# Optimization experiments

Measured on AMD Instinct MI355X. Metric: run time of the kernel, lower is better.

## Reference

```python
import jax, jax.numpy as jnp
import numpy as np

S, B, I, H, O = 4096, 64, 14, 256, 1


def _lstm_layer(xs, W_ih, W_hh, b_ih, b_hh, h, c):
    # Precompute input contribution for all timesteps in one big GEMM.
    # xs: [S, B, D_in] -> pre: [S, B, 4H]  (PyTorch gate order: i, f, g, o)
    pre = jnp.einsum('sbd,gd->sbg', xs, W_ih) + b_ih + b_hh

    def step(carry, px):
        h, c = carry
        gates = px + h @ W_hh.T  # [B, 4H]
        i, f, g, o = jnp.split(gates, 4, axis=-1)
        i = jax.nn.sigmoid(i)
        f = jax.nn.sigmoid(f)
        g = jnp.tanh(g)
        o = jax.nn.sigmoid(o)
        c = f * c + i * g
        h = o * jnp.tanh(c)
        return (h, c), h

    (_, _), hs = jax.lax.scan(step, (h, c), pre)
    return hs  # [S, B, H]


def setup_inputs() -> dict:
    key = jax.random.key(0)
    ks = jax.random.split(key, 14)
    s = 1.0 / np.sqrt(H)  # PyTorch LSTM init scale
    u = lambda k, shape: jax.random.uniform(k, shape, jnp.float32, -s, s)
    return {
        'x': jax.random.normal(ks[0], (S, B, I), jnp.float32),
        'h0': jax.random.normal(ks[1], (2, B, H), jnp.float32),
        'c0': jax.random.normal(ks[2], (2, B, H), jnp.float32),
        'W_ih0': u(ks[3], (4 * H, I)),
        'W_hh0': u(ks[4], (4 * H, H)),
        'b_ih0': u(ks[5], (4 * H,)),
        'b_hh0': u(ks[6], (4 * H,)),
        'W_ih1': u(ks[7], (4 * H, H)),
        'W_hh1': u(ks[8], (4 * H, H)),
        'b_ih1': u(ks[9], (4 * H,)),
        'b_hh1': u(ks[10], (4 * H,)),
        'W_fc': u(ks[11], (O, H)),
        'b_fc': u(ks[12], (O,)),
    }


def reference(x, h0, c0, W_ih0, W_hh0, b_ih0, b_hh0,
              W_ih1, W_hh1, b_ih1, b_hh1, W_fc, b_fc):
    hs0 = _lstm_layer(x, W_ih0, W_hh0, b_ih0, b_hh0, h0[0], c0[0])
    # dropout=0.4 between layers applies only in train mode; eval reference -> identity
    hs1 = _lstm_layer(hs0, W_ih1, W_hh1, b_ih1, b_hh1, h0[1], c0[1])
    out = jax.nn.relu(hs1)
    return out @ W_fc.T + b_fc  # [S, B, O]
```

## Files before the change

kernel.cpp:

```cpp
#include <hip/hip_runtime.h>


#define S_LEN 4096
#define BATCH 64
#define IN_DIM 14
#define HID 256
#define GATES 1024
#define K0 288
#define LDA0 296
#define K1 512
#define LDA1 520
#define GST 260

typedef _Float16 half8 __attribute__((ext_vector_type(8)));
typedef float f32x4 __attribute__((ext_vector_type(4)));
typedef unsigned long long u64;
typedef unsigned int u32;

__device__ __forceinline__ float sigf(float z) { return 1.0f / (1.0f + __expf(-z)); }
__device__ __forceinline__ float tanhf2(float z) { return 2.0f / (1.0f + __expf(-2.0f * z)) - 1.0f; }

__device__ __forceinline__ u32 packh2(float a, float b) {
    union { _Float16 h[2]; u32 u; } q;
    q.h[0] = (_Float16)a; q.h[1] = (_Float16)b;
    return q.u;
}

__device__ __forceinline__ u64 ld64_c(const u64* p) {
    u64 r;
    asm volatile("global_load_dwordx2 %0, %1, off sc0 sc1\n\ts_waitcnt vmcnt(0)"
                 : "=&v"(r) : "v"(p) : "memory");
    return r;
}
__device__ __forceinline__ void st64_c(u64* p, u64 v) {
    asm volatile("global_store_dwordx2 %0, %1, off sc0 sc1" :: "v"(p), "v"(v) : "memory");
}
__device__ __forceinline__ u32 ld32_c(const u32* p) {
    u32 r;
    asm volatile("global_load_dword %0, %1, off sc0 sc1\n\ts_waitcnt vmcnt(0)"
                 : "=&v"(r) : "v"(p) : "memory");
    return r;
}
__device__ __forceinline__ void st32_c(u32* p, u32 v) {
    asm volatile("global_store_dword %0, %1, off sc0 sc1" :: "v"(p), "v"(v) : "memory");
}
__device__ __forceinline__ void ld64x3_c(const u64* p0, const u64* p1, const u64* p2,
                                         u64& r0, u64& r1, u64& r2) {
    asm volatile(
        "global_load_dwordx2 %0, %3, off sc0 sc1\n\t"
        "global_load_dwordx2 %1, %4, off sc0 sc1\n\t"
        "global_load_dwordx2 %2, %5, off sc0 sc1\n\t"
        "s_waitcnt vmcnt(0)"
        : "=&v"(r0), "=&v"(r1), "=&v"(r2)
        : "v"(p0), "v"(p1), "v"(p2)
        : "memory");
}
__device__ __forceinline__ void ld64x7_c(
    const u64* a0, const u64* a1, const u64* a2, const u64* a3,
    const u64* p0, const u64* p1, const u64* p2,
    u64& q0, u64& q1, u64& q2, u64& q3, u64& v0, u64& v1, u64& v2) {
    asm volatile(
        "global_load_dwordx2 %0, %7, off sc0 sc1\n\t"
        "global_load_dwordx2 %1, %8, off sc0 sc1\n\t"
        "global_load_dwordx2 %2, %9, off sc0 sc1\n\t"
        "global_load_dwordx2 %3, %10, off sc0 sc1\n\t"
        "global_load_dwordx2 %4, %11, off sc0 sc1\n\t"
        "global_load_dwordx2 %5, %12, off sc0 sc1\n\t"
        "global_load_dwordx2 %6, %13, off sc0 sc1\n\t"
        "s_waitcnt vmcnt(0)"
        : "=&v"(q0), "=&v"(q1), "=&v"(q2), "=&v"(q3), "=&v"(v0), "=&v"(v1), "=&v"(v2)
        : "v"(a0), "v"(a1), "v"(a2), "v"(a3), "v"(p0), "v"(p1), "v"(p2)
        : "memory");
}

__global__ void prep_weights(const float* __restrict__ Wih0, const float* __restrict__ Whh0,
                             const float* __restrict__ bih0, const float* __restrict__ bhh0,
                             const float* __restrict__ Wih1, const float* __restrict__ Whh1,
                             const float* __restrict__ bih1, const float* __restrict__ bhh1,
                             _Float16* __restrict__ wcat0, _Float16* __restrict__ wcat1,
                             float* __restrict__ b0, float* __restrict__ b1) {
    int idx0 = blockIdx.x * blockDim.x + threadIdx.x;
    int stride = gridDim.x * blockDim.x;
    for (int i = idx0; i < GATES * K0; i += stride) {
        int n = i / K0, k = i % K0;
        float v = 0.f;
        if (k < HID) v = Whh0[n * HID + k];
        else if (k < HID + IN_DIM) v = Wih0[n * IN_DIM + (k - HID)];
        wcat0[i] = (_Float16)v;
    }
    for (int i = idx0; i < GATES * K1; i += stride) {
        int n = i / K1, k = i % K1;
        float v = (k < HID) ? Whh1[n * HID + k] : Wih1[n * HID + (k - HID)];
        wcat1[i] = (_Float16)v;
    }
    for (int i = idx0; i < GATES; i += stride) {
        b0[i] = bih0[i] + bhh0[i];
        b1[i] = bih1[i] + bhh1[i];
    }
}

__global__ __launch_bounds__(512) void lstm_scan(
    const float* __restrict__ x, const float* __restrict__ h0g, const float* __restrict__ c0g,
    const _Float16* __restrict__ wcat0, const _Float16* __restrict__ wcat1,
    const float* __restrict__ b0, const float* __restrict__ b1,
    const float* __restrict__ wfc, const float* __restrict__ bfc,
    u64* __restrict__ h0ring, u64* __restrict__ h1ring,
    u32* __restrict__ prog, float* __restrict__ out, int R0) {
    const int bi = blockIdx.x;
    const int x7 = bi & 7;
    const int g = x7 >> 1;
    const int sub = ((x7 & 1) << 2) | (bi >> 3);
    const int L = sub >> 2;
    const int j = sub & 3;

    const int tid = threadIdx.x;
    const int w = tid >> 6;
    const int lane = tid & 63;
    const int quad = lane >> 4;
    const int col = lane & 15;
    const int c0b = g * 16;
    const int pm = tid & 15;
    const int iu = tid >> 4;
    const int pu = iu * 2;
    const int gm = tid >> 5;
    const int gu = tid & 31;

    __shared__ __align__(16) _Float16 Ash[16 * LDA1];
    __shared__ float Gsh[16 * GST];
    __shared__ float WfS[HID];
    __shared__ u32 OwnH[512];

    u64* h0w = h0ring + (size_t)g * R0 * 2048;
    u64* h1w = h1ring + (size_t)g * 4 * 2048;
    const int R0m = R0 - 1;

    int peer[3];
    { int c = 0; for (int p = 0; p < 4; ++p) if (p != j) peer[c++] = p; }

    int gbudget = 1 << 24;

    if (L == 0) {
        half8 wr[2][K0 / 32];
        float bs[2];
#pragma unroll
        for (int tt = 0; tt < 2; ++tt) {
            int t = w + 8 * tt;
            int n = (t >> 2) * 256 + j * 64 + (t & 3) * 16 + col;
            bs[tt] = b0[n];
            const _Float16* wp = wcat0 + (size_t)n * K0 + quad * 8;
#pragma unroll
            for (int kk = 0; kk < K0 / 32; ++kk) wr[tt][kk] = *(const half8*)(wp + kk * 32);
        }
        float cs0 = c0g[(size_t)(c0b + pm) * HID + j * 64 + pu];
        float cs1 = c0g[(size_t)(c0b + pm) * HID + j * 64 + pu + 1];
        {
            int m = tid >> 5, cw = tid & 31;
            const float* hp = h0g + (size_t)(c0b + m) * HID + cw * 8;
            half8 hv;
#pragma unroll
            for (int q2 = 0; q2 < 8; ++q2) hv[q2] = (_Float16)hp[q2];
            *(half8*)&Ash[m * LDA0 + cw * 8] = hv;
            if (cw >= IN_DIM) Ash[m * LDA0 + HID + cw] = (_Float16)0.f;
        }
        const int xm = tid / IN_DIM, xd = tid - xm * IN_DIM;
        if (tid < 16 * IN_DIM)
            Ash[xm * LDA0 + HID + xd] = (_Float16)x[(size_t)(c0b + xm) * IN_DIM + xd];
        __syncthreads();

        for (int s = 0; s < S_LEN; ++s) {
            float xpre = 0.f;
            if (tid < 16 * IN_DIM && s + 1 < S_LEN)
                xpre = x[((size_t)(s + 1) * BATCH + c0b + xm) * IN_DIM + xd];
            if (w == 0 && lane < 4 && (s & 7) == 0 && s + 10 > R0) {
                const u32* np = prog + g * 4 + lane;
                int tgt = s + 10 - R0;
                while ((int)ld32_c(np) < tgt && --gbudget > 0) __builtin_amdgcn_s_sleep(4);
            }
            if (s > 0) {
                const u64* base = h0w + (size_t)((s - 1) & R0m) * 2048;
                const u64* p0 = base + peer[0] * 512 + tid;
                const u64* p1 = base + peer[1] * 512 + tid;
                const u64* p2 = base + peer[2] * 512 + tid;
                u64 v0, v1, v2;
                ld64x3_c(p0, p1, p2, v0, v1, v2);
                const u32 tg = (u32)s;
                while ((u32)(v0 >> 32) != tg && --gbudget > 0) v0 = ld64_c(p0);
                while ((u32)(v1 >> 32) != tg && --gbudget > 0) v1 = ld64_c(p1);
                while ((u32)(v2 >> 32) != tg && --gbudget > 0) v2 = ld64_c(p2);
                *(u32*)&Ash[gm * LDA0 + peer[0] * 64 + 2 * gu] = (u32)v0;
                *(u32*)&Ash[gm * LDA0 + peer[1] * 64 + 2 * gu] = (u32)v1;
                *(u32*)&Ash[gm * LDA0 + peer[2] * 64 + 2 * gu] = (u32)v2;
            }
            __syncthreads();
            f32x4 acc0 = {bs[0], bs[0], bs[0], bs[0]};
            f32x4 acc1 = {bs[1], bs[1], bs[1], bs[1]};
#pragma unroll
            for (int kk = 0; kk < K0 / 32; ++kk) {
                half8 av = *(const half8*)&Ash[col * LDA0 + kk * 32 + quad * 8];
                acc0 = __builtin_amdgcn_mfma_f32_16x16x32_f16(av, wr[0][kk], acc0, 0, 0, 0);
                acc1 = __builtin_amdgcn_mfma_f32_16x16x32_f16(av, wr[1][kk], acc1, 0, 0, 0);
            }
#pragma unroll
            for (int r = 0; r < 4; ++r) {
                Gsh[(quad * 4 + r) * GST + w * 16 + col] = acc0[r];
                Gsh[(quad * 4 + r) * GST + (w + 8) * 16 + col] = acc1[r];
            }
            __syncthreads();
            {
                float iv = sigf(Gsh[pm * GST + pu]);
                float fv = sigf(Gsh[pm * GST + 64 + pu]);
                float gv = tanhf2(Gsh[pm * GST + 128 + pu]);
                float ov = sigf(Gsh[pm * GST + 192 + pu]);
                cs0 = fv * cs0 + iv * gv;
                float ha = ov * tanhf2(cs0);
                iv = sigf(Gsh[pm * GST + pu + 1]);
                fv = sigf(Gsh[pm * GST + 64 + pu + 1]);
                gv = tanhf2(Gsh[pm * GST + 128 + pu + 1]);
                ov = sigf(Gsh[pm * GST + 192 + pu + 1]);
                cs1 = fv * cs1 + iv * gv;
                float hb = ov * tanhf2(cs1);
                u32 hw = packh2(ha, hb);
                *(u32*)&Ash[pm * LDA0 + j * 64 + pu] = hw;
                st64_c(h0w + (size_t)(s & R0m) * 2048 + j * 512 + (pm * 32 + iu),
                       (u64)hw | ((u64)(u32)(s + 1) << 32));
            }
            if (tid < 16 * IN_DIM && s + 1 < S_LEN)
                Ash[xm * LDA0 + HID + xd] = (_Float16)xpre;
            __syncthreads();
        }
    } else {
        half8 wr[2][K1 / 32];
        float bs[2];
#pragma unroll
        for (int tt = 0; tt < 2; ++tt) {
            int t = w + 8 * tt;
            int n = (t >> 2) * 256 + j * 64 + (t & 3) * 16 + col;
            bs[tt] = b1[n];
            const _Float16* wp = wcat1 + (size_t)n * K1 + quad * 8;
#pragma unroll
            for (int kk = 0; kk < K1 / 32; ++kk) wr[tt][kk] = *(const half8*)(wp + kk * 32);
        }
        for (int i = tid; i < HID; i += 512) WfS[i] = wfc[i];
        const float bfcv = bfc[0];
        float cs0 = c0g[(size_t)(BATCH + c0b + pm) * HID + j * 64 + pu];
        float cs1 = c0g[(size_t)(BATCH + c0b + pm) * HID + j * 64 + pu + 1];
        {
            int m = tid >> 5, cw = tid & 31;
            const float* hp = h0g + (size_t)(BATCH + c0b + m) * HID + cw * 8;
            half8 hv;
#pragma unroll
            for (int q2 = 0; q2 < 8; ++q2) hv[q2] = (_Float16)hp[q2];
            *(half8*)&Ash[m * LDA1 + cw * 8] = hv;
        }
        u32* progself = prog + g * 4 + j;
        __syncthreads();

        for (int s = 0; s <= S_LEN; ++s) {
            if (w == 7 && s >= 2) {
                int m = 4 * j + quad;
                float fa = 0.f;
#pragma unroll
                for (int k16 = 0; k16 < 16; ++k16) {
                    float hv = (float)Ash[m * LDA1 + col + 16 * k16];
                    fa += fmaxf(hv, 0.f) * WfS[col + 16 * k16];
                }
#pragma unroll
                for (int off = 1; off < 16; off <<= 1) fa += __shfl_xor(fa, off, 16);
                if (col == 0) out[(size_t)(s - 2) * BATCH + c0b + m] = fa + bfcv;
            }
            const u64* hb = h0w + (size_t)((s < S_LEN ? s : 0) & R0m) * 2048;
            const u64* a0 = hb + tid;
            const u64* a1 = hb + 512 + tid;
            const u64* a2 = hb + 1024 + tid;
            const u64* a3 = hb + 1536 + tid;
            const u64* pb = h1w + (size_t)(((s > 0 ? s : 1) - 1) & 3) * 2048;
            const u64* p0 = pb + peer[0] * 512 + tid;
            const u64* p1 = pb + peer[1] * 512 + tid;
            const u64* p2 = pb + peer[2] * 512 + tid;
            u64 q0, q1, q2, q3, v0, v1, v2;
            ld64x7_c(a0, a1, a2, a3, p0, p1, p2, q0, q1, q2, q3, v0, v1, v2);
            if (s < S_LEN) {
                const u32 tg = (u32)(s + 1);
                while ((u32)(q0 >> 32) != tg && --gbudget > 0) q0 = ld64_c(a0);
                while ((u32)(q1 >> 32) != tg && --gbudget > 0) q1 = ld64_c(a1);
                while ((u32)(q2 >> 32) != tg && --gbudget > 0) q2 = ld64_c(a2);
                while ((u32)(q3 >> 32) != tg && --gbudget > 0) q3 = ld64_c(a3);
            }
            if (s > 0) {
                const u32 tg = (u32)s;
                while ((u32)(v0 >> 32) != tg && --gbudget > 0) v0 = ld64_c(p0);
                while ((u32)(v1 >> 32) != tg && --gbudget > 0) v1 = ld64_c(p1);
                while ((u32)(v2 >> 32) != tg && --gbudget > 0) v2 = ld64_c(p2);
            }
            __syncthreads();
            if (s > 0) {
                *(u32*)&Ash[gm * LDA1 + peer[0] * 64 + 2 * gu] = (u32)v0;
                *(u32*)&Ash[gm * LDA1 + peer[1] * 64 + 2 * gu] = (u32)v1;
                *(u32*)&Ash[gm * LDA1 + peer[2] * 64 + 2 * gu] = (u32)v2;
                *(u32*)&Ash[gm * LDA1 + j * 64 + 2 * gu] = OwnH[tid];
            }
            if (s < S_LEN) {
                *(u32*)&Ash[gm * LDA1 + HID + 0 * 64 + 2 * gu] = (u32)q0;
                *(u32*)&Ash[gm * LDA1 + HID + 1 * 64 + 2 * gu] = (u32)q1;
                *(u32*)&Ash[gm * LDA1 + HID + 2 * 64 + 2 * gu] = (u32)q2;
                *(u32*)&Ash[gm * LDA1 + HID + 3 * 64 + 2 * gu] = (u32)q3;
            }
            __syncthreads();
            if (s == S_LEN) {
                if (w == 7) {
                    int m = 4 * j + quad;
                    float fa = 0.f;
#pragma unroll
                    for (int k16 = 0; k16 < 16; ++k16) {
                        float hv = (float)Ash[m * LDA1 + col + 16 * k16];
                        fa += fmaxf(hv, 0.f) * WfS[col + 16 * k16];
                    }
#pragma unroll
                    for (int off = 1; off < 16; off <<= 1) fa += __shfl_xor(fa, off, 16);
                    if (col == 0) out[(size_t)(S_LEN - 1) * BATCH + c0b + m] = fa + bfcv;
                }
                break;
            }
            f32x4 acc0 = {bs[0], bs[0], bs[0], bs[0]};
            f32x4 acc1 = {bs[1], bs[1], bs[1], bs[1]};
#pragma unroll
            for (int kk = 0; kk < K1 / 32; ++kk) {
                half8 av = *(const half8*)&Ash[col * LDA1 + kk * 32 + quad * 8];
                acc0 = __builtin_amdgcn_mfma_f32_16x16x32_f16(av, wr[0][kk], acc0, 0, 0, 0);
                acc1 = __builtin_amdgcn_mfma_f32_16x16x32_f16(av, wr[1][kk], acc1, 0, 0, 0);
            }
#pragma unroll
            for (int r = 0; r < 4; ++r) {
                Gsh[(quad * 4 + r) * GST + w * 16 + col] = acc0[r];
                Gsh[(quad * 4 + r) * GST + (w + 8) * 16 + col] = acc1[r];
            }
            __syncthreads();
            {
                float iv = sigf(Gsh[pm * GST + pu]);
                float fv = sigf(Gsh[pm * GST + 64 + pu]);
                float gv = tanhf2(Gsh[pm * GST + 128 + pu]);
                float ov = sigf(Gsh[pm * GST + 192 + pu]);
                cs0 = fv * cs0 + iv * gv;
                float ha = ov * tanhf2(cs0);
                iv = sigf(Gsh[pm * GST + pu + 1]);
                fv = sigf(Gsh[pm * GST + 64 + pu + 1]);
                gv = tanhf2(Gsh[pm * GST + 128 + pu + 1]);
                ov = sigf(Gsh[pm * GST + 192 + pu + 1]);
                cs1 = fv * cs1 + iv * gv;
                float hb = ov * tanhf2(cs1);
                u32 hw = packh2(ha, hb);
                OwnH[pm * 32 + iu] = hw;
                st64_c(h1w + (size_t)(s & 3) * 2048 + j * 512 + (pm * 32 + iu),
                       (u64)hw | ((u64)(u32)(s + 1) << 32));
            }
            if ((s & 7) == 7 && tid == 0) st32_c(progself, (u32)(s + 1));
            __syncthreads();
        }
    }
}

extern "C" void kernel_launch(void* const* d_in, const int* in_sizes, int n_in,
                              void* d_out, int out_size, void* d_ws, size_t ws_size,
                              hipStream_t stream) {
    const float* x    = (const float*)d_in[0];
    const float* h0   = (const float*)d_in[1];
    const float* c0   = (const float*)d_in[2];
    const float* Wih0 = (const float*)d_in[3];
    const float* Whh0 = (const float*)d_in[4];
    const float* bih0 = (const float*)d_in[5];
    const float* bhh0 = (const float*)d_in[6];
    const float* Wih1 = (const float*)d_in[7];
    const float* Whh1 = (const float*)d_in[8];
    const float* bih1 = (const float*)d_in[9];
    const float* bhh1 = (const float*)d_in[10];
    const float* Wfc  = (const float*)d_in[11];
    const float* bfc  = (const float*)d_in[12];
    float* out = (float*)d_out;

    char* ws = (char*)d_ws;
    constexpr size_t OFF_WCAT0 = 0;
    constexpr size_t SZ_WCAT0 = (size_t)GATES * K0 * 2;
    constexpr size_t OFF_WCAT1 = OFF_WCAT0 + SZ_WCAT0;
    constexpr size_t SZ_WCAT1 = (size_t)GATES * K1 * 2;
    constexpr size_t OFF_B0 = OFF_WCAT1 + SZ_WCAT1;
    constexpr size_t OFF_B1 = OFF_B0 + 4096;
    constexpr size_t OFF_PROG = OFF_B1 + 4096;
    constexpr size_t OFF_H1R = OFF_PROG + 4096;
    constexpr size_t SZ_H1R = (size_t)4 * 4 * 2048 * 8;
    constexpr size_t OFF_H0R = OFF_H1R + SZ_H1R;

    _Float16* wcat0 = (_Float16*)(ws + OFF_WCAT0);
    _Float16* wcat1 = (_Float16*)(ws + OFF_WCAT1);
    float* b0 = (float*)(ws + OFF_B0);
    float* b1 = (float*)(ws + OFF_B1);
    u32* prog = (u32*)(ws + OFF_PROG);
    u64* h1ring = (u64*)(ws + OFF_H1R);

    int R0 = 128;
    while (OFF_H0R + (size_t)4 * R0 * 2048 * 8 > ws_size && R0 > 16) R0 >>= 1;
    u64* h0ring = (u64*)(ws + OFF_H0R);

    hipMemsetAsync(ws + OFF_PROG, 0,
                   (OFF_H0R - OFF_PROG) + (size_t)4 * R0 * 2048 * 8, stream);
    prep_weights<<<256, 256, 0, stream>>>(Wih0, Whh0, bih0, bhh0, Wih1, Whh1, bih1, bhh1,
                                          wcat0, wcat1, b0, b1);
    lstm_scan<<<32, 512, 0, stream>>>(x, h0, c0, wcat0, wcat1, b0, b1, Wfc, bfc,
                                      h0ring, h1ring, prog, out, R0);
}
```

Measured before the change: 10.74 ms.

## Batch spin-wait polls and drop trailing barrier in LSTM step loop

Replaces the per-peer sequential spin loops with combined polls that reload all three (layer 0) or all seven (layer 1) flag-tagged values in one batched load until every tag matches. This is meant to cut the serialized round-trip latency of polling each peer in turn. It also removes the end-of-step __syncthreads in layer 0, pads the gate scratch stride to 261 to avoid LDS bank conflicts, and lowers the timeout budget. Dropping the barrier risks a race between the next step's Ash writes and the current step's reads.

```diff
diff --git a/kernel.cpp b/kernel.cpp
--- a/kernel.cpp
+++ b/kernel.cpp
@@ -10,7 +10,7 @@
 #define LDA0 296
 #define K1 512
 #define LDA1 520
-#define GST 260
+#define GST 261
 
 typedef _Float16 half8 __attribute__((ext_vector_type(8)));
 typedef float f32x4 __attribute__((ext_vector_type(4)));
@@ -26,15 +26,6 @@
     return q.u;
 }
 
-__device__ __forceinline__ u64 ld64_c(const u64* p) {
-    u64 r;
-    asm volatile("global_load_dwordx2 %0, %1, off sc0 sc1\n\ts_waitcnt vmcnt(0)"
-                 : "=&v"(r) : "v"(p) : "memory");
-    return r;
-}
-__device__ __forceinline__ void st64_c(u64* p, u64 v) {
-    asm volatile("global_store_dwordx2 %0, %1, off sc0 sc1" :: "v"(p), "v"(v) : "memory");
-}
 __device__ __forceinline__ u32 ld32_c(const u32* p) {
     u32 r;
     asm volatile("global_load_dword %0, %1, off sc0 sc1\n\ts_waitcnt vmcnt(0)"
@@ -43,6 +34,9 @@
 }
 __device__ __forceinline__ void st32_c(u32* p, u32 v) {
     asm volatile("global_store_dword %0, %1, off sc0 sc1" :: "v"(p), "v"(v) : "memory");
+}
+__device__ __forceinline__ void st64_c(u64* p, u64 v) {
+    asm volatile("global_store_dwordx2 %0, %1, off sc0 sc1" :: "v"(p), "v"(v) : "memory");
 }
 __device__ __forceinline__ void ld64x3_c(const u64* p0, const u64* p1, const u64* p2,
                                          u64& r0, u64& r1, u64& r2) {
@@ -137,7 +131,7 @@
     int peer[3];
     { int c = 0; for (int p = 0; p < 4; ++p) if (p != j) peer[c++] = p; }
 
-    int gbudget = 1 << 24;
+    int gbudget = 1 << 22;
 
     if (L == 0) {
         half8 wr[2][K0 / 32];
@@ -184,9 +178,9 @@
                 u64 v0, v1, v2;
                 ld64x3_c(p0, p1, p2, v0, v1, v2);
                 const u32 tg = (u32)s;
-                while ((u32)(v0 >> 32) != tg && --gbudget > 0) v0 = ld64_c(p0);
-                while ((u32)(v1 >> 32) != tg && --gbudget > 0) v1 = ld64_c(p1);
-                while ((u32)(v2 >> 32) != tg && --gbudget > 0) v2 = ld64_c(p2);
+                while ((((u32)(v0 >> 32) != tg) | ((u32)(v1 >> 32) != tg) |
+                        ((u32)(v2 >> 32) != tg)) && --gbudget > 0)
+                    ld64x3_c(p0, p1, p2, v0, v1, v2);
                 *(u32*)&Ash[gm * LDA0 + peer[0] * 64 + 2 * gu] = (u32)v0;
                 *(u32*)&Ash[gm * LDA0 + peer[1] * 64 + 2 * gu] = (u32)v1;
                 *(u32*)&Ash[gm * LDA0 + peer[2] * 64 + 2 * gu] = (u32)v2;
@@ -226,7 +220,6 @@
             }
             if (tid < 16 * IN_DIM && s + 1 < S_LEN)
                 Ash[xm * LDA0 + HID + xd] = (_Float16)xpre;
-            __syncthreads();
         }
     } else {
         half8 wr[2][K1 / 32];
@@ -279,18 +272,19 @@
             const u64* p2 = pb + peer[2] * 512 + tid;
             u64 q0, q1, q2, q3, v0, v1, v2;
             ld64x7_c(a0, a1, a2, a3, p0, p1, p2, q0, q1, q2, q3, v0, v1, v2);
-            if (s < S_LEN) {
-                const u32 tg = (u32)(s + 1);
-                while ((u32)(q0 >> 32) != tg && --gbudget > 0) q0 = ld64_c(a0);
-                while ((u32)(q1 >> 32) != tg && --gbudget > 0) q1 = ld64_c(a1);
-                while ((u32)(q2 >> 32) != tg && --gbudget > 0) q2 = ld64_c(a2);
-                while ((u32)(q3 >> 32) != tg && --gbudget > 0) q3 = ld64_c(a3);
-            }
-            if (s > 0) {
-                const u32 tg = (u32)s;
-                while ((u32)(v0 >> 32) != tg && --gbudget > 0) v0 = ld64_c(p0);
-                while ((u32)(v1 >> 32) != tg && --gbudget > 0) v1 = ld64_c(p1);
-                while ((u32)(v2 >> 32) != tg && --gbudget > 0) v2 = ld64_c(p2);
+            {
+                const u32 tgq = (u32)(s + 1), tgv = (u32)s;
+                for (;;) {
+                    bool bad = false;
+                    if (s < S_LEN)
+                        bad |= ((u32)(q0 >> 32) != tgq) | ((u32)(q1 >> 32) != tgq) |
+                               ((u32)(q2 >> 32) != tgq) | ((u32)(q3 >> 32) != tgq);
+                    if (s > 0)
+                        bad |= ((u32)(v0 >> 32) != tgv) | ((u32)(v1 >> 32) != tgv) |
+                               ((u32)(v2 >> 32) != tgv);
+                    if (!bad || --gbudget <= 0) break;
+                    ld64x7_c(a0, a1, a2, a3, p0, p1, p2, q0, q1, q2, q3, v0, v1, v2);
+                }
             }
             __syncthreads();
             if (s > 0) {
```

Result: faster. 10.26 ms (-4.5%).
